# Performance work log

Hardware: AMD Instinct MI355X
Metric: run time of the kernel (lower is better)

Reference implementation:

```python
import jax, jax.numpy as jnp
import numpy as np

D_MODEL = 512
NUM_HEADS = 8
D_HEAD = D_MODEL // NUM_HEADS


def setup_inputs() -> dict:
    key = jax.random.key(0)
    ks = jax.random.split(key, 16)
    B, S, D, H, dh = 8, 1024, D_MODEL, NUM_HEADS, D_HEAD
    s = 1.0 / np.sqrt(D)
    return {
        "query": jax.random.normal(ks[0], (B, S, D), jnp.float32),
        "key": jax.random.normal(ks[1], (B, S, D), jnp.float32),
        "value": jax.random.normal(ks[2], (B, S, D), jnp.float32),
        "pos_emb": jax.random.normal(ks[3], (B, S, D), jnp.float32),
        "Wq": jax.random.normal(ks[4], (D, D), jnp.float32) * s,
        "bq": jnp.zeros((D,), jnp.float32),
        "Wk": jax.random.normal(ks[5], (D, D), jnp.float32) * s,
        "bk": jnp.zeros((D,), jnp.float32),
        "Wv": jax.random.normal(ks[6], (D, D), jnp.float32) * s,
        "bv": jnp.zeros((D,), jnp.float32),
        "Wpos": jax.random.normal(ks[7], (D, D), jnp.float32) * s,  # pos_proj has no bias
        "Wo": jax.random.normal(ks[8], (D, D), jnp.float32) * s,
        "bo": jnp.zeros((D,), jnp.float32),
        "u_bias": jax.random.normal(ks[9], (H, dh), jnp.float32) * 0.02,
        "v_bias": jax.random.normal(ks[10], (H, dh), jnp.float32) * 0.02,
    }


def _rel_shift(x):
    # x: [B, H, S, S] -> Transformer-XL relative shift
    B, H, S1, S2 = x.shape
    x = jnp.pad(x, ((0, 0), (0, 0), (0, 0), (1, 0)))  # zero col at front
    x = x.reshape(B, H, S2 + 1, S1)[:, :, 1:, :]
    return x.reshape(B, H, S1, S2)


def reference(query, key, value, pos_emb, Wq, bq, Wk, bk, Wv, bv, Wpos, Wo, bo, u_bias, v_bias):
    B, S, D = query.shape
    H, dh = NUM_HEADS, D_HEAD
    q = (query @ Wq + bq).reshape(B, S, H, dh)      # [B,S,H,dh]
    k = (key @ Wk + bk).reshape(B, S, H, dh)
    v = (value @ Wv + bv).reshape(B, S, H, dh)
    p = (pos_emb @ Wpos).reshape(B, S, H, dh)
    content_score = jnp.einsum('bqhd,bkhd->bhqk', q + u_bias, k)
    pos_score = _rel_shift(jnp.einsum('bqhd,bkhd->bhqk', q + v_bias, p))
    score = (content_score + pos_score) / jnp.sqrt(jnp.float32(D))
    attn = jax.nn.softmax(score, axis=-1)
    ctx = jnp.einsum('bhqk,bkhd->bqhd', attn, v).reshape(B, S, D)
    return ctx @ Wo + bo
```

## Files before the change

kernel.cpp:

```cpp
#include <hip/hip_runtime.h>
#include <hip/hip_bf16.h>

typedef unsigned short u16;
typedef unsigned int u32;
typedef __attribute__((ext_vector_type(4))) float f32x4;
typedef __attribute__((ext_vector_type(8))) short s16x8;
typedef __attribute__((ext_vector_type(4))) short s16x4;

#define DEV static __device__ __forceinline__

DEV u16 f2bf(float f){ return __builtin_bit_cast(u16, __float2bfloat16(f)); }
DEV float bf2f(u16 v){ union{u32 u;float f;}x; x.u = ((u32)v)<<16; return x.f; }
DEV float bitsf(u32 u){ union{u32 u;float f;}x; x.u = u; return x.f; }

DEV f32x4 MF(s16x8 a, s16x8 b, f32x4 c){ return __builtin_amdgcn_mfma_f32_16x16x32_bf16(a,b,c,0,0,0); }

DEV s16x8 frag64(const u16* lds, int row, int slot){
  return *(const s16x8*)(lds + row*64 + ((slot ^ (row&7))<<3));
}

__global__ __launch_bounds__(256) void k_prep(
  const float* __restrict__ Wq, const float* __restrict__ Wk, const float* __restrict__ Wv,
  const float* __restrict__ Wp, const float* __restrict__ Wo, u16* __restrict__ WT)
{
  const int bx = blockIdx.x; const int mat = bx>>6, tile = bx&63;
  const float* W = (mat==0)?Wq:(mat==1)?Wk:(mat==2)?Wv:(mat==3)?Wp:Wo;
  u16* dst = WT + mat*262144;
  const int k0 = (tile>>3)<<6, n0 = (tile&7)<<6;
  __shared__ u16 L[64*68];
  const int t = threadIdx.x;
#pragma unroll
  for (int i=0;i<4;i++){
    int id = t + 256*i; int row = id>>4, c4 = (id&15)<<2;
    float4 v = *(const float4*)(W + (k0+row)*512 + n0 + c4);
    s16x4 o; o[0]=(short)f2bf(v.x); o[1]=(short)f2bf(v.y); o[2]=(short)f2bf(v.z); o[3]=(short)f2bf(v.w);
    *(s16x4*)(L + row*68 + c4) = o;
  }
  __syncthreads();
#pragma unroll
  for (int i=0;i<2;i++){
    int id = t + 256*i; int nl = id>>3, slot = id&7;
    s16x8 v;
#pragma unroll
    for (int j=0;j<8;j++) v[j] = (short)L[(slot*8+j)*68 + nl];
    *(s16x8*)(dst + (n0+nl)*512 + k0 + slot*8) = v;
  }
}

__global__ __launch_bounds__(256,2) void k_proj(
  const float* __restrict__ Xq, const float* __restrict__ Xk,
  const float* __restrict__ Xv, const float* __restrict__ Xp,
  const u16* __restrict__ WT,
  const float* __restrict__ bq, const float* __restrict__ bk, const float* __restrict__ bv,
  const float* __restrict__ ub, const float* __restrict__ vb,
  u16* __restrict__ Qu, u16* __restrict__ Qv, u16* __restrict__ Kb,
  u16* __restrict__ Pb, u16* __restrict__ Vt)
{
  const int Lb = blockIdx.x;
  const int xcd = Lb & 7, li = Lb >> 3;
  const int n0  = (li & 3) * 128;
  const int job = (li >> 2) & 3;
  const int m0  = (xcd*8 + (li >> 4)) * 128;
  const float* X = (job==0)?Xq:(job==1)?Xk:(job==2)?Xp:Xv;
  const int wsel = (job==0)?0:(job==1)?1:(job==2)?3:2;
  const u16* W = WT + wsel*262144;
  __shared__ u16 As[128*64];
  __shared__ u16 Bs[128*64];
  const int t = threadIdx.x, lane = t&63, w = t>>6;
  const int wm = w&1, wn = w>>1;
  f32x4 acc[4][4];
#pragma unroll
  for (int i=0;i<4;i++)
#pragma unroll
    for (int j=0;j<4;j++) acc[i][j] = (f32x4){0.f,0.f,0.f,0.f};

  for (int kt=0; kt<8; ++kt){
    const int k0 = kt*64;
    __syncthreads();
#pragma unroll
    for (int i=0;i<8;i++){
      int id = t + 256*i; int row = id>>4; int c4 = (id&15)<<2;
      float4 v = *(const float4*)(X + (m0+row)*512 + k0 + c4);
      s16x4 o; o[0]=(short)f2bf(v.x); o[1]=(short)f2bf(v.y); o[2]=(short)f2bf(v.z); o[3]=(short)f2bf(v.w);
      *(s16x4*)(As + row*64 + ((((c4>>3)^(row&7))<<3) + (c4&4))) = o;
    }
#pragma unroll
    for (int i=0;i<4;i++){
      int id = t + 256*i; int row = id>>3, slot = id&7;
      s16x8 v = *(const s16x8*)(W + (n0+row)*512 + k0 + slot*8);
      *(s16x8*)(Bs + row*64 + ((slot^(row&7))<<3)) = v;
    }
    __syncthreads();
#pragma unroll
    for (int kk=0;kk<2;kk++){
      const int slotk = kk*4 + (lane>>4);
      s16x8 xf[4], wf[4];
#pragma unroll
      for (int j=0;j<4;j++){ int r = wm*64 + j*16 + (lane&15); xf[j] = frag64(As, r, slotk); }
#pragma unroll
      for (int i=0;i<4;i++){ int r = wn*64 + i*16 + (lane&15); wf[i] = frag64(Bs, r, slotk); }
      if (job != 3){
#pragma unroll
        for (int i=0;i<4;i++)
#pragma unroll
          for (int j=0;j<4;j++) acc[i][j] = MF(wf[i], xf[j], acc[i][j]);
      } else {
#pragma unroll
        for (int i=0;i<4;i++)
#pragma unroll
          for (int j=0;j<4;j++) acc[i][j] = MF(xf[i], wf[j], acc[i][j]);
      }
    }
  }

  const int b = m0>>10;
  if (job != 3){
#pragma unroll
    for (int i=0;i<4;i++){
      const int n = n0 + wn*64 + i*16 + ((lane>>4)<<2);
      const int hh = n>>6, d = n&63;
      f32x4 b1 = {0.f,0.f,0.f,0.f}, b2 = {0.f,0.f,0.f,0.f};
      if (job==0){
        f32x4 q4 = *(const f32x4*)(bq+n); f32x4 u4 = *(const f32x4*)(ub+n); f32x4 v4 = *(const f32x4*)(vb+n);
        b1 = q4 + u4; b2 = q4 + v4;
      } else if (job==1){
        b1 = *(const f32x4*)(bk+n);
      }
#pragma unroll
      for (int j=0;j<4;j++){
        const int m = m0 + wm*64 + j*16 + (lane&15);
        const int s = m&1023;
        const int off = ((b*8+hh)*1024 + s)*64 + d;
        f32x4 a = acc[i][j];
        s16x4 o1;
#pragma unroll
        for (int r=0;r<4;r++) o1[r] = (short)f2bf(a[r]+b1[r]);
        if (job==0){
          *(s16x4*)(Qu+off) = o1;
          s16x4 o2;
#pragma unroll
          for (int r=0;r<4;r++) o2[r] = (short)f2bf(a[r]+b2[r]);
          *(s16x4*)(Qv+off) = o2;
        } else if (job==1) *(s16x4*)(Kb+off) = o1;
        else               *(s16x4*)(Pb+off) = o1;
      }
    }
  } else {
#pragma unroll
    for (int j=0;j<4;j++){
      const int n = n0 + wn*64 + j*16 + (lane&15);
      const int hh = n>>6, d = n&63;
      const float bvn = bv[n];
#pragma unroll
      for (int i=0;i<4;i++){
        const int m = m0 + wm*64 + i*16 + ((lane>>4)<<2);
        const int s = m&1023;
        f32x4 a = acc[i][j];
        s16x4 o;
#pragma unroll
        for (int r=0;r<4;r++) o[r] = (short)f2bf(a[r]+bvn);
        *(s16x4*)(Vt + ((b*8+hh)*64 + d)*1024 + s) = o;
      }
    }
  }
}

#define SC_SLOT(q, slot) ((((slot)) & ~7) | ((((slot))&7) ^ ((q)&7)))

__global__ __launch_bounds__(512,2) void k_attn(
  const u16* __restrict__ Qu, const u16* __restrict__ Qv,
  const u16* __restrict__ Kb, const u16* __restrict__ Pb,
  const u16* __restrict__ Vt, u16* __restrict__ Ctx)
{
  const int Lb = blockIdx.x;
  const int xcd = Lb & 7, li = Lb >> 3;
  const int bh = xcd*8 + (li>>5);
  const int qb = li & 31;
  const int q0 = qb*32;
  const u16* Qu_ = Qu + bh*65536;
  const u16* Qv_ = Qv + bh*65536;
  const u16* Kb_ = Kb + bh*65536;
  const u16* Pb_ = Pb + bh*65536;
  const u16* Vt_ = Vt + bh*65536;
  u16* Ctx_ = Ctx + bh*65536;
  __shared__ u16 sc[33*1024];
  __shared__ u16 Ts[4096];
  __shared__ float pmax[512];
  __shared__ float stats[32];
  const int t = threadIdx.x, lane = t&63, w = t>>6;
  const int l15 = lane&15, lg = lane>>4;
  const int qband = w&1, sub = w>>1;
  const int qi = qband*16 + l15;
  const int q  = q0 + qi;
  const int srow = t>>3, sslot = t&7;
  u16* tsw = Ts + srow*64 + ((sslot^(srow&7))<<3);
  const u16* srcP = Pb_ + srow*64 + sslot*8;
  const u16* srcK = Kb_ + srow*64 + sslot*8;
  const u16* srcV = Vt_ + srow*1024 + sslot*8;

  const int priBand = w>>2, jtp = w&3;
  s16x8 qvp[2], qvb2[2];
#pragma unroll
  for (int kk=0;kk<2;kk++){
    qvp[kk]  = *(const s16x8*)(Qv_ + (q0 + priBand*16 + l15)*64 + (kk*4+lg)*8);
    int r2 = q0 + 17 + l15; if (r2 > 1023) r2 = 1023;
    qvb2[kk] = *(const s16x8*)(Qv_ + r2*64 + (kk*4+lg)*8);
  }

  {
    s16x8 p0 = *(const s16x8*)(srcP);
    s16x8 p1 = *(const s16x8*)(srcP + 4096);
#pragma unroll
    for (int u=0; u<16; ++u){
      __syncthreads();
      *(s16x8*)tsw = p0;
      p0 = p1;
      if (u+2<16) p1 = *(const s16x8*)(srcP + (u+2)*4096);
      __syncthreads();
      {
        f32x4 ps = {0.f,0.f,0.f,0.f};
#pragma unroll
        for (int kk=0;kk<2;kk++){
          s16x8 pf = frag64(Ts, jtp*16 + l15, kk*4+lg);
          ps = MF(pf, qvp[kk], ps);
        }
        const int prow = priBand*16 + l15;
        const int j0 = u*64 + jtp*16 + lg*4;
        s16x4 o;
#pragma unroll
        for (int r=0;r<4;r++) o[r] = (short)f2bf(ps[r]);
        *(s16x4*)(sc + prow*1024 + ((((j0>>2) ^ ((prow&15)<<1)))<<2)) = o;
      }
      if ((u&1) == (w>>2)){
        f32x4 ps = {0.f,0.f,0.f,0.f};
#pragma unroll
        for (int kk=0;kk<2;kk++){
          s16x8 pf = frag64(Ts, (w&3)*16 + l15, kk*4+lg);
          ps = MF(pf, qvb2[kk], ps);
        }
        if (l15 == 15){
          const int j0 = u*64 + (w&3)*16 + lg*4;
          s16x4 o;
#pragma unroll
          for (int r=0;r<4;r++) o[r] = (short)f2bf(ps[r]);
          *(s16x4*)(sc + 32*1024 + ((j0>>2)<<2)) = o;
        }
      }
    }
  }

  __syncthreads();

  u32 stash[32];
#pragma unroll
  for (int kt=0; kt<16; ++kt){
#pragma unroll
    for (int rp=0; rp<2; ++rp){
      u32 wv = 0;
#pragma unroll
      for (int hh=0; hh<2; ++hh){
        const int k = kt*64 + sub*16 + lg*4 + rp*2 + hh;
        const int above = (k > q) ? 1 : 0;
        int jj = above ? (k - q - 2) : (1023 - q + k);
        const bool zero = (k == q+1);
        if (jj < 0) jj = 0;
        const int row = qi + above;
        const int addr = row*1024 + ((((jj>>2) ^ ((row&15)<<1)))<<2) + (jj&3);
        u32 v = zero ? 0u : (u32)sc[addr];
        wv |= v << (16*hh);
      }
      stash[kt*2+rp] = wv;
    }
  }

  s16x8 qfu[2];
#pragma unroll
  for (int kk=0;kk<2;kk++)
    qfu[kk] = *(const s16x8*)(Qu_ + q*64 + (kk*4+lg)*8);

  float rmax = -1e30f;
  {
    s16x8 k0r = *(const s16x8*)(srcK);
    s16x8 k1r = *(const s16x8*)(srcK + 4096);
#pragma unroll
    for (int kt=0; kt<16; ++kt){
      __syncthreads();
      *(s16x8*)tsw = k0r;
      k0r = k1r;
      if (kt+2<16) k1r = *(const s16x8*)(srcK + (kt+2)*4096);
      __syncthreads();
      f32x4 a = {0.f,0.f,0.f,0.f};
#pragma unroll
      for (int kk=0;kk<2;kk++){
        s16x8 kf = frag64(Ts, sub*16 + l15, kk*4+lg);
        a = MF(kf, qfu[kk], a);
      }
      const int kb2 = kt*64 + sub*16 + lg*4;
      const u32 w0 = stash[kt*2], w1 = stash[kt*2+1];
      const float v0 = a[0] + bitsf(w0<<16);
      const float v1 = a[1] + bitsf(w0 & 0xffff0000u);
      const float v2 = a[2] + bitsf(w1<<16);
      const float v3 = a[3] + bitsf(w1 & 0xffff0000u);
      rmax = fmaxf(rmax, fmaxf(fmaxf(v0,v1), fmaxf(v2,v3)));
      s16x4 o;
      o[0]=(short)f2bf(v0); o[1]=(short)f2bf(v1);
      o[2]=(short)f2bf(v2); o[3]=(short)f2bf(v3);
      *(s16x4*)(sc + qi*1024 + SC_SLOT(qi, kb2>>3)*8 + (kb2&4)) = o;
    }
  }
  pmax[qi*16 + sub*4 + lg] = rmax;

  __syncthreads();

  {
    const int row = t>>4, c = t&15;
    float mx = pmax[row*16 + c];
    mx = fmaxf(mx, __shfl_xor(mx,1));
    mx = fmaxf(mx, __shfl_xor(mx,2));
    mx = fmaxf(mx, __shfl_xor(mx,4));
    mx = fmaxf(mx, __shfl_xor(mx,8));
    const float S2 = 0.063762029f;
    const float nm = -mx * S2;
    float sum = 0.f;
#pragma unroll
    for (int i=0;i<8;i++){
      const int slot = c + 16*i;
      u16* p = sc + row*1024 + SC_SLOT(row,slot)*8;
      s16x8 v = *(const s16x8*)p;
      s16x8 o;
#pragma unroll
      for (int j2=0;j2<8;j2++){
        float e = exp2f(__builtin_fmaf(bf2f((u16)v[j2]), S2, nm));
        sum += e; o[j2] = (short)f2bf(e);
      }
      *(s16x8*)p = o;
    }
    sum += __shfl_xor(sum,1); sum += __shfl_xor(sum,2);
    sum += __shfl_xor(sum,4); sum += __shfl_xor(sum,8);
    if (c==0) stats[row] = 1.0f/sum;
  }

  f32x4 accC = {0.f,0.f,0.f,0.f};
  const int dtile = w>>1;
  {
    s16x8 v0r = *(const s16x8*)(srcV);
    s16x8 v1r = *(const s16x8*)(srcV + 64);
#pragma unroll
    for (int kt=0; kt<16; ++kt){
      __syncthreads();
      *(s16x8*)tsw = v0r;
      v0r = v1r;
      if (kt+2<16) v1r = *(const s16x8*)(srcV + (kt+2)*64);
      __syncthreads();
#pragma unroll
      for (int kk=0;kk<2;kk++){
        const int slotk = kk*4 + lg;
        s16x8 vf = frag64(Ts, dtile*16 + l15, slotk);
        const int slot = kt*8 + slotk;
        s16x8 pfr = *(const s16x8*)(sc + qi*1024 + SC_SLOT(qi,slot)*8);
        accC = MF(vf, pfr, accC);
      }
    }
  }
  {
    const float inv = stats[qi];
    const int d0 = dtile*16 + lg*4;
    s16x4 o;
#pragma unroll
    for (int r=0;r<4;r++) o[r] = (short)f2bf(accC[r]*inv);
    *(s16x4*)(Ctx_ + (q0+qi)*64 + d0) = o;
  }
}

__global__ __launch_bounds__(256,2) void k_out(
  const u16* __restrict__ Ctx, const u16* __restrict__ WT,
  const float* __restrict__ bo, float* __restrict__ Out)
{
  const u16* W = WT + 4*262144;
  const int m0 = blockIdx.y*128, n0 = blockIdx.x*128;
  const int b = m0>>10, s0 = m0&1023;
  __shared__ u16 As[128*64];
  __shared__ u16 Bs[128*64];
  const int t = threadIdx.x, lane = t&63, w = t>>6;
  const int wm = w&1, wn = w>>1;
  f32x4 acc[4][4];
#pragma unroll
  for (int i=0;i<4;i++)
#pragma unroll
    for (int j=0;j<4;j++) acc[i][j] = (f32x4){0.f,0.f,0.f,0.f};

  for (int kt=0; kt<8; ++kt){
    const int k0 = kt*64, hh = kt;
    __syncthreads();
#pragma unroll
    for (int i=0;i<4;i++){
      int id = t + 256*i; int row = id>>3, slot = id&7;
      s16x8 v = *(const s16x8*)(Ctx + ((b*8+hh)*1024 + s0 + row)*64 + slot*8);
      *(s16x8*)(As + row*64 + ((slot^(row&7))<<3)) = v;
    }
#pragma unroll
    for (int i=0;i<4;i++){
      int id = t + 256*i; int row = id>>3, slot = id&7;
      s16x8 v = *(const s16x8*)(W + (n0+row)*512 + k0 + slot*8);
      *(s16x8*)(Bs + row*64 + ((slot^(row&7))<<3)) = v;
    }
    __syncthreads();
#pragma unroll
    for (int kk=0;kk<2;kk++){
      const int slotk = kk*4 + (lane>>4);
      s16x8 xf[4], wf[4];
#pragma unroll
      for (int j=0;j<4;j++){ int r = wm*64 + j*16 + (lane&15); xf[j] = frag64(As, r, slotk); }
#pragma unroll
      for (int i=0;i<4;i++){ int r = wn*64 + i*16 + (lane&15); wf[i] = frag64(Bs, r, slotk); }
#pragma unroll
      for (int i=0;i<4;i++)
#pragma unroll
        for (int j=0;j<4;j++) acc[i][j] = MF(wf[i], xf[j], acc[i][j]);
    }
  }
#pragma unroll
  for (int i=0;i<4;i++){
    const int n = n0 + wn*64 + i*16 + ((lane>>4)<<2);
    f32x4 bo4 = *(const f32x4*)(bo + n);
#pragma unroll
    for (int j=0;j<4;j++){
      const int m = m0 + wm*64 + j*16 + (lane&15);
      f32x4 o = acc[i][j] + bo4;
      *(f32x4*)(Out + m*512 + n) = o;
    }
  }
}

extern "C" void kernel_launch(void* const* d_in, const int* in_sizes, int n_in,
                              void* d_out, int out_size, void* d_ws, size_t ws_size,
                              hipStream_t stream)
{
  const float* query = (const float*)d_in[0];
  const float* key   = (const float*)d_in[1];
  const float* value = (const float*)d_in[2];
  const float* pos   = (const float*)d_in[3];
  const float* Wq = (const float*)d_in[4];
  const float* bq = (const float*)d_in[5];
  const float* Wk = (const float*)d_in[6];
  const float* bk = (const float*)d_in[7];
  const float* Wv = (const float*)d_in[8];
  const float* bv = (const float*)d_in[9];
  const float* Wp = (const float*)d_in[10];
  const float* Wo = (const float*)d_in[11];
  const float* bo = (const float*)d_in[12];
  const float* ub = (const float*)d_in[13];
  const float* vb = (const float*)d_in[14];
  float* Out = (float*)d_out;

  u16* ws  = (u16*)d_ws;
  u16* WT  = ws;
  u16* Qu  = ws + 1310720;
  u16* Qv  = Qu + 4194304;
  u16* Kb  = Qv + 4194304;
  u16* Pb  = Kb + 4194304;
  u16* Vt  = Pb + 4194304;
  u16* Ctx = Vt + 4194304;

  k_prep<<<dim3(320),  dim3(256), 0, stream>>>(Wq,Wk,Wv,Wp,Wo,WT);
  k_proj<<<dim3(1024), dim3(256), 0, stream>>>(query,key,value,pos,WT,bq,bk,bv,ub,vb,Qu,Qv,Kb,Pb,Vt);
  k_attn<<<dim3(2048), dim3(512), 0, stream>>>(Qu,Qv,Kb,Pb,Vt,Ctx);
  k_out<<<dim3(4,64),  dim3(256), 0, stream>>>(Ctx,WT,bo,Out);
}
```

Baseline: 177.6 us.

## Fuse rel-shift gather into QK loop and keep scores in registers for softmax

The separate pre-pass that stashed relative-shifted positional scores is removed; the shifted gather from LDS now happens inside the QK^T loop, right after the MFMAs. The combined scores stay in registers as packed bf16 and softmax exponentiation runs on those registers. Exponentials are written back to the same LDS layout, and row max and row sum are reduced through shared memory with extra barriers. s_setprio is also raised around MFMA sections. This removes an LDS write/read round trip of the score matrix, at the cost of two more block barriers and higher register pressure.

After: 241.9 us. +36.2%, slower.

```diff
diff --git a/kernel.cpp b/kernel.cpp
--- a/kernel.cpp
+++ b/kernel.cpp
@@ -186,6 +186,7 @@
   __shared__ u16 sc[33*1024];
   __shared__ u16 Ts[4096];
   __shared__ float pmax[512];
+  __shared__ float mrow[32];
   __shared__ float stats[32];
   const int t = threadIdx.x, lane = t&63, w = t>>6;
   const int l15 = lane&15, lg = lane>>4;
@@ -219,11 +220,13 @@
       __syncthreads();
       {
         f32x4 ps = {0.f,0.f,0.f,0.f};
+        __builtin_amdgcn_s_setprio(1);
 #pragma unroll
         for (int kk=0;kk<2;kk++){
           s16x8 pf = frag64(Ts, jtp*16 + l15, kk*4+lg);
           ps = MF(pf, qvp[kk], ps);
         }
+        __builtin_amdgcn_s_setprio(0);
         const int prow = priBand*16 + l15;
         const int j0 = u*64 + jtp*16 + lg*4;
         s16x4 o;
@@ -233,11 +236,13 @@
       }
       if ((u&1) == (w>>2)){
         f32x4 ps = {0.f,0.f,0.f,0.f};
+        __builtin_amdgcn_s_setprio(1);
 #pragma unroll
         for (int kk=0;kk<2;kk++){
           s16x8 pf = frag64(Ts, (w&3)*16 + l15, kk*4+lg);
           ps = MF(pf, qvb2[kk], ps);
         }
+        __builtin_amdgcn_s_setprio(0);
         if (l15 == 15){
           const int j0 = u*64 + (w&3)*16 + lg*4;
           s16x4 o;
@@ -251,61 +256,47 @@
 
   __syncthreads();
 
-  u32 stash[32];
-#pragma unroll
-  for (int kt=0; kt<16; ++kt){
-#pragma unroll
-    for (int rp=0; rp<2; ++rp){
-      u32 wv = 0;
-#pragma unroll
-      for (int hh=0; hh<2; ++hh){
-        const int k = kt*64 + sub*16 + lg*4 + rp*2 + hh;
+  s16x8 qfu[2];
+#pragma unroll
+  for (int kk=0;kk<2;kk++)
+    qfu[kk] = *(const s16x8*)(Qu_ + q*64 + (kk*4+lg)*8);
+
+  float rmax = -1e30f;
+  u32 scr[32];
+  {
+    s16x8 k0r = *(const s16x8*)(srcK);
+    s16x8 k1r = *(const s16x8*)(srcK + 4096);
+#pragma unroll
+    for (int kt=0; kt<16; ++kt){
+      __syncthreads();
+      *(s16x8*)tsw = k0r;
+      k0r = k1r;
+      if (kt+2<16) k1r = *(const s16x8*)(srcK + (kt+2)*4096);
+      __syncthreads();
+      f32x4 a = {0.f,0.f,0.f,0.f};
+      __builtin_amdgcn_s_setprio(1);
+#pragma unroll
+      for (int kk=0;kk<2;kk++){
+        s16x8 kf = frag64(Ts, sub*16 + l15, kk*4+lg);
+        a = MF(kf, qfu[kk], a);
+      }
+      __builtin_amdgcn_s_setprio(0);
+      const int kb2 = kt*64 + sub*16 + lg*4;
+      float vv[4];
+#pragma unroll
+      for (int r=0;r<4;r++){
+        const int k = kb2 + r;
         const int above = (k > q) ? 1 : 0;
         int jj = above ? (k - q - 2) : (1023 - q + k);
-        const bool zero = (k == q+1);
         if (jj < 0) jj = 0;
         const int row = qi + above;
         const int addr = row*1024 + ((((jj>>2) ^ ((row&15)<<1)))<<2) + (jj&3);
-        u32 v = zero ? 0u : (u32)sc[addr];
-        wv |= v << (16*hh);
-      }
-      stash[kt*2+rp] = wv;
-    }
-  }
-
-  s16x8 qfu[2];
-#pragma unroll
-  for (int kk=0;kk<2;kk++)
-    qfu[kk] = *(const s16x8*)(Qu_ + q*64 + (kk*4+lg)*8);
-
-  float rmax = -1e30f;
-  {
-    s16x8 k0r = *(const s16x8*)(srcK);
-    s16x8 k1r = *(const s16x8*)(srcK + 4096);
-#pragma unroll
-    for (int kt=0; kt<16; ++kt){
-      __syncthreads();
-      *(s16x8*)tsw = k0r;
-      k0r = k1r;
-      if (kt+2<16) k1r = *(const s16x8*)(srcK + (kt+2)*4096);
-      __syncthreads();
-      f32x4 a = {0.f,0.f,0.f,0.f};
-#pragma unroll
-      for (int kk=0;kk<2;kk++){
-        s16x8 kf = frag64(Ts, sub*16 + l15, kk*4+lg);
-        a = MF(kf, qfu[kk], a);
-      }
-      const int kb2 = kt*64 + sub*16 + lg*4;
-      const u32 w0 = stash[kt*2], w1 = stash[kt*2+1];
-      const float v0 = a[0] + bitsf(w0<<16);
-      const float v1 = a[1] + bitsf(w0 & 0xffff0000u);
-      const float v2 = a[2] + bitsf(w1<<16);
-      const float v3 = a[3] + bitsf(w1 & 0xffff0000u);
-      rmax = fmaxf(rmax, fmaxf(fmaxf(v0,v1), fmaxf(v2,v3)));
-      s16x4 o;
-      o[0]=(short)f2bf(v0); o[1]=(short)f2bf(v1);
-      o[2]=(short)f2bf(v2); o[3]=(short)f2bf(v3);
-      *(s16x4*)(sc + qi*1024 + SC_SLOT(qi, kb2>>3)*8 + (kb2&4)) = o;
+        const float posf = (k == q+1) ? 0.f : bf2f(sc[addr]);
+        vv[r] = a[r] + posf;
+      }
+      rmax = fmaxf(rmax, fmaxf(fmaxf(vv[0],vv[1]), fmaxf(vv[2],vv[3])));
+      scr[kt*2]   = ((u32)f2bf(vv[0])) | (((u32)f2bf(vv[1]))<<16);
+      scr[kt*2+1] = ((u32)f2bf(vv[2])) | (((u32)f2bf(vv[3]))<<16);
     }
   }
   pmax[qi*16 + sub*4 + lg] = rmax;
@@ -319,25 +310,38 @@
     mx = fmaxf(mx, __shfl_xor(mx,2));
     mx = fmaxf(mx, __shfl_xor(mx,4));
     mx = fmaxf(mx, __shfl_xor(mx,8));
+    if (c==0) mrow[row] = mx;
+  }
+  __syncthreads();
+
+  {
     const float S2 = 0.063762029f;
-    const float nm = -mx * S2;
+    const float nm = -mrow[qi] * S2;
     float sum = 0.f;
 #pragma unroll
-    for (int i=0;i<8;i++){
-      const int slot = c + 16*i;
-      u16* p = sc + row*1024 + SC_SLOT(row,slot)*8;
-      s16x8 v = *(const s16x8*)p;
-      s16x8 o;
-#pragma unroll
-      for (int j2=0;j2<8;j2++){
-        float e = exp2f(__builtin_fmaf(bf2f((u16)v[j2]), S2, nm));
-        sum += e; o[j2] = (short)f2bf(e);
-      }
-      *(s16x8*)p = o;
-    }
-    sum += __shfl_xor(sum,1); sum += __shfl_xor(sum,2);
-    sum += __shfl_xor(sum,4); sum += __shfl_xor(sum,8);
-    if (c==0) stats[row] = 1.0f/sum;
+    for (int kt=0; kt<16; ++kt){
+      const int kb2 = kt*64 + sub*16 + lg*4;
+      const u32 w0 = scr[kt*2], w1 = scr[kt*2+1];
+      const float e0 = exp2f(__builtin_fmaf(bitsf(w0<<16),          S2, nm));
+      const float e1 = exp2f(__builtin_fmaf(bitsf(w0 & 0xffff0000u),S2, nm));
+      const float e2 = exp2f(__builtin_fmaf(bitsf(w1<<16),          S2, nm));
+      const float e3 = exp2f(__builtin_fmaf(bitsf(w1 & 0xffff0000u),S2, nm));
+      sum += (e0+e1)+(e2+e3);
+      s16x4 o;
+      o[0]=(short)f2bf(e0); o[1]=(short)f2bf(e1);
+      o[2]=(short)f2bf(e2); o[3]=(short)f2bf(e3);
+      *(s16x4*)(sc + qi*1024 + SC_SLOT(qi, kb2>>3)*8 + (kb2&4)) = o;
+    }
+    pmax[qi*16 + sub*4 + lg] = sum;
+  }
+  __syncthreads();
+
+  {
+    const int row = t>>4, c = t&15;
+    float s = pmax[row*16 + c];
+    s += __shfl_xor(s,1); s += __shfl_xor(s,2);
+    s += __shfl_xor(s,4); s += __shfl_xor(s,8);
+    if (c==0) stats[row] = 1.0f/s;
   }
 
   f32x4 accC = {0.f,0.f,0.f,0.f};
@@ -352,6 +356,7 @@
       v0r = v1r;
       if (kt+2<16) v1r = *(const s16x8*)(srcV + (kt+2)*64);
       __syncthreads();
+      __builtin_amdgcn_s_setprio(1);
 #pragma unroll
       for (int kk=0;kk<2;kk++){
         const int slotk = kk*4 + lg;
@@ -360,6 +365,7 @@
         s16x8 pfr = *(const s16x8*)(sc + qi*1024 + SC_SLOT(qi,slot)*8);
         accC = MF(vf, pfr, accC);
       }
+      __builtin_amdgcn_s_setprio(0);
     }
   }
   {
```
